# Kernel tuning notes

Measured on AMD Instinct MI355X. Metric: run time of the kernel, lower is better.

The kernel has to match this reference:

```python
import jax, jax.numpy as jnp
import numpy as np

N_NODES = 20000
N_EDGES = 640000
N_TRIP = 1000000
C = 128          # channels
E = 64           # expansion_features
CUTOFF = 5.0
LOG2 = float(np.log(2.0))


def ssp(x):
    # ShiftedSoftplus
    return jax.nn.softplus(x) - LOG2


def setup_inputs() -> dict:
    key = jax.random.key(0)
    ks = jax.random.split(key, 12)
    features = jax.random.normal(ks[0], (N_NODES, C), dtype=jnp.float32)
    neighbour_distances = jax.random.uniform(ks[1], (N_EDGES,), dtype=jnp.float32) * (1.2 * CUTOFF)
    neighbour_list = jax.random.randint(ks[2], (2, N_EDGES), 0, N_NODES, dtype=jnp.int32)
    triplet_idxs = jax.random.randint(ks[3], (N_TRIP, 3), 0, N_NODES, dtype=jnp.int32)
    angles = jax.random.uniform(ks[4], (N_TRIP,), dtype=jnp.float32) * np.pi
    r_ij = jax.random.uniform(ks[5], (N_TRIP,), dtype=jnp.float32) * CUTOFF
    r_ik = jax.random.uniform(ks[6], (N_TRIP,), dtype=jnp.float32) * CUTOFF
    # learned parameters (Linear layers without bias; stored [in, out])
    W_pre = jax.random.normal(ks[7], (C, C), dtype=jnp.float32) / np.sqrt(C)
    W2b1 = jax.random.normal(ks[8], (E, E), dtype=jnp.float32) / np.sqrt(E)
    W2b2 = jax.random.normal(ks[9], (E, C), dtype=jnp.float32) / np.sqrt(E)
    W3b1 = jax.random.normal(ks[10], (3, C // 2), dtype=jnp.float32) / np.sqrt(3.0)
    W3b2 = jax.random.normal(ks[11], (C // 2, C), dtype=jnp.float32) / np.sqrt(C // 2)
    W_post = jax.random.normal(jax.random.fold_in(key, 99), (C, C), dtype=jnp.float32) / np.sqrt(C)
    return {
        "features": features,
        "neighbour_distances": neighbour_distances,
        "neighbour_list": neighbour_list,
        "triplet_idxs": triplet_idxs,
        "angles": angles,
        "r_ij": r_ij,
        "r_ik": r_ik,
        "W_pre": W_pre,
        "W2b1": W2b1,
        "W2b2": W2b2,
        "W3b1": W3b1,
        "W3b2": W3b2,
        "W_post": W_post,
    }


def reference(features, neighbour_distances, neighbour_list, triplet_idxs,
              angles, r_ij, r_ik, W_pre, W2b1, W2b2, W3b1, W3b2, W_post):
    # 1) pre-linear
    h = features @ W_pre                                   # [N, C]

    # 2) radial basis (Gaussian smearing) with smooth cosine cutoff envelope
    centers = jnp.linspace(0.0, CUTOFF, E, dtype=jnp.float32)  # [E]
    width = CUTOFF / E
    gamma = 1.0 / (2.0 * width * width)
    d = neighbour_distances[:, None]                       # [n_edges, 1]
    rb = jnp.exp(-gamma * (d - centers) ** 2)              # [n_edges, E]
    cutoff_mask = (neighbour_distances < CUTOFF).astype(jnp.float32)
    cutoff_values = 0.5 * (1.0 + jnp.cos(np.pi * neighbour_distances / CUTOFF))
    rb = rb * (cutoff_values * cutoff_mask)[:, None]       # fused envelope

    # 3) two-body messages: gather neighbour node features, modulate by radial MLP
    neighbor_h = h[neighbour_list[1]]                      # [n_edges, C]
    two_body = neighbor_h * (ssp(rb @ W2b1) @ W2b2)        # [n_edges, C]

    # 4) three-body messages: angular MLP on (r_ij, r_ik, cos(angle)),
    #    gather node features at triplet_idxs[:,1], scatter-add into edge slots
    tbf = jnp.stack([r_ij, r_ik, jnp.cos(angles)], axis=-1)  # [n_trip, 3]
    w3 = ssp(tbf @ W3b1) @ W3b2                              # [n_trip, C]
    msgs = h[triplet_idxs[:, 1]] * w3                        # [n_trip, C]
    edge_msgs = jnp.zeros_like(two_body).at[triplet_idxs[:, 1]].add(msgs)

    # 5) aggregate messages over neighbours (to central atom = neighbour_list[0])
    messages = two_body + edge_msgs
    agg = jax.ops.segment_sum(messages, neighbour_list[0], num_segments=N_NODES)

    # 6) post-linear
    return agg @ W_post
```

## Files before the change

### kernel.cpp

```cpp
#include <hip/hip_runtime.h>
#include <hip/hip_fp16.h>
#include <math.h>

#define TID threadIdx.x

typedef ushort u16x8 __attribute__((ext_vector_type(8)));
typedef unsigned char uchar;

static constexpr int NN = 20000;
static constexpr int NE = 640000;
static constexpr int NT = 1000000;
static constexpr int C = 128;
static constexpr int E = 64;
static constexpr int LUTN = 4104;
static constexpr int NBKT = 313;
static constexpr int NB2 = 512;
static constexpr int CHE2 = 1250;
static constexpr int CHT2 = 1954;
static constexpr float CUT = 5.0f;
static constexpr float LN2 = 0.69314718055994530942f;

__device__ __forceinline__ float ssp(float x) {
    return fmaxf(x, 0.0f) + __logf(1.0f + __expf(-fabsf(x))) - LN2;
}

__device__ __forceinline__ ushort f2bf(float x) {
    uint u = __float_as_uint(x);
    return (ushort)((u + 0x7FFFu + ((u >> 16) & 1u)) >> 16);
}

__device__ __forceinline__ float bf2f(ushort u) {
    return __uint_as_float((uint)u << 16);
}

__device__ __forceinline__ float h2f(uint bits) {
    return __half2float(__ushort_as_half((ushort)(bits & 0xFFFFu)));
}

__global__ __launch_bounds__(256) void k_gemm16f(const float* __restrict__ A,
                                                 const float* __restrict__ W,
                                                 float* __restrict__ out, int nrows) {
    __shared__ ushort wB[C * C];
    __shared__ float aL[16][132];
    for (int i = TID; i < C * C / 4; i += 256) {
        float4 w4 = ((const float4*)W)[i];
        ushort4 u = {f2bf(w4.x), f2bf(w4.y), f2bf(w4.z), f2bf(w4.w)};
        ((ushort4*)wB)[i] = u;
    }
    const int base = blockIdx.x * 16;
    for (int i = TID; i < 512; i += 256) {
        int r = base + (i >> 5);
        float4 v = (r < nrows) ? ((const float4*)A)[(size_t)r * 32 + (i & 31)]
                               : (float4){0.f, 0.f, 0.f, 0.f};
        *(float4*)&aL[i >> 5][(i & 31) << 2] = v;
    }
    __syncthreads();
    const int rg = TID >> 4;
    const int c8 = (TID & 15) << 3;
    float acc[8] = {0.f, 0.f, 0.f, 0.f, 0.f, 0.f, 0.f, 0.f};
    #pragma unroll 8
    for (int k = 0; k < C; ++k) {
        float a = aL[rg][k];
        u16x8 wv = *(const u16x8*)&wB[k * C + c8];
        #pragma unroll
        for (int j = 0; j < 8; ++j) acc[j] = fmaf(a, bf2f(wv[j]), acc[j]);
    }
    int r = base + rg;
    if (r < nrows) {
        float4 o0 = {acc[0], acc[1], acc[2], acc[3]};
        float4 o1 = {acc[4], acc[5], acc[6], acc[7]};
        *(float4*)&out[(size_t)r * C + c8] = o0;
        *(float4*)&out[(size_t)r * C + c8 + 4] = o1;
    }
}

__global__ __launch_bounds__(256) void k_gemm16b(const float* __restrict__ A,
                                                 const float* __restrict__ W,
                                                 ushort* __restrict__ outB, int nrows) {
    __shared__ ushort wB[C * C];
    __shared__ float aL[16][132];
    for (int i = TID; i < C * C / 4; i += 256) {
        float4 w4 = ((const float4*)W)[i];
        ushort4 u = {f2bf(w4.x), f2bf(w4.y), f2bf(w4.z), f2bf(w4.w)};
        ((ushort4*)wB)[i] = u;
    }
    const int base = blockIdx.x * 16;
    for (int i = TID; i < 512; i += 256) {
        int r = base + (i >> 5);
        float4 v = (r < nrows) ? ((const float4*)A)[(size_t)r * 32 + (i & 31)]
                               : (float4){0.f, 0.f, 0.f, 0.f};
        *(float4*)&aL[i >> 5][(i & 31) << 2] = v;
    }
    __syncthreads();
    const int rg = TID >> 4;
    const int c8 = (TID & 15) << 3;
    float acc[8] = {0.f, 0.f, 0.f, 0.f, 0.f, 0.f, 0.f, 0.f};
    #pragma unroll 8
    for (int k = 0; k < C; ++k) {
        float a = aL[rg][k];
        u16x8 wv = *(const u16x8*)&wB[k * C + c8];
        #pragma unroll
        for (int j = 0; j < 8; ++j) acc[j] = fmaf(a, bf2f(wv[j]), acc[j]);
    }
    int r = base + rg;
    if (r < nrows) {
        u16x8 u;
        #pragma unroll
        for (int j = 0; j < 8; ++j) u[j] = f2bf(acc[j]);
        *(u16x8*)&outB[(size_t)r * C + c8] = u;
    }
}

__global__ __launch_bounds__(256) void k_lut(const float* __restrict__ W2b1,
                                             const float* __restrict__ W2b2,
                                             ushort* __restrict__ lutB,
                                             float2* __restrict__ spLut) {
    if (blockIdx.x == (LUTN + 7) / 8) {
        for (int e = TID; e < 512; e += 256) {
            float t0 = (float)e * (1.0f / 32.0f);
            float t1 = (float)(e + 1) * (1.0f / 32.0f);
            float v0 = log1pf(__expf(-t0));
            float v1 = log1pf(__expf(-t1));
            spLut[e] = make_float2(v0, v1 - v0);
        }
        return;
    }
    __shared__ float w1[E * E];
    __shared__ float w2[E * C];
    __shared__ float rbL[8][E];
    __shared__ float hid[8][E];
    for (int i = TID; i < E * E; i += 256) w1[i] = W2b1[i];
    for (int i = TID; i < E * C; i += 256) w2[i] = W2b2[i];
    const int jj = TID & 63;
    const int esA = TID >> 6;
    const int eg = TID >> 5;
    const int c4 = (TID & 31) << 2;
    const float gamma = 81.92f;
    const float cstep = CUT / 63.0f;
    const float delta = CUT / 4096.0f;
    const int base = blockIdx.x * 8;
    __syncthreads();
    #pragma unroll
    for (int s = 0; s < 2; ++s) {
        int es = esA + 4 * s;
        float d = (float)(base + es) * delta;
        float cv = (d < CUT) ? 0.5f * (1.0f + __cosf((float)M_PI * d / CUT)) : 0.0f;
        float dd = d - (float)jj * cstep;
        rbL[es][jj] = __expf(-gamma * dd * dd) * cv;
    }
    __syncthreads();
    #pragma unroll
    for (int s = 0; s < 2; ++s) {
        int es = esA + 4 * s;
        float a = 0.f;
        #pragma unroll 16
        for (int k = 0; k < E; ++k)
            a = fmaf(rbL[es][k], w1[k * E + jj], a);
        hid[es][jj] = ssp(a);
    }
    __syncthreads();
    float4 o = {0.f, 0.f, 0.f, 0.f};
    #pragma unroll
    for (int j = 0; j < E; ++j) {
        float t = hid[eg][j];
        const float4 w4 = *(const float4*)&w2[j * C + c4];
        o.x = fmaf(t, w4.x, o.x);
        o.y = fmaf(t, w4.y, o.y);
        o.z = fmaf(t, w4.z, o.z);
        o.w = fmaf(t, w4.w, o.w);
    }
    int row = base + eg;
    if (row < LUTN) {
        ushort4 u = {f2bf(o.x), f2bf(o.y), f2bf(o.z), f2bf(o.w)};
        *(ushort4*)&lutB[(size_t)row * C + c4] = u;
    }
}

__global__ __launch_bounds__(256) void k_bcount(const int* __restrict__ nl0,
                                                const int* __restrict__ tidx,
                                                uchar* __restrict__ cntE,
                                                uchar* __restrict__ cntT) {
    __shared__ int h[NBKT];
    const int b = blockIdx.x;
    for (int i = TID; i < NBKT; i += 256) h[i] = 0;
    __syncthreads();
    const int e0 = b * CHE2, e1 = min(e0 + CHE2, NE);
    for (int i = e0 + TID; i < e1; i += 256) atomicAdd(&h[nl0[i] >> 6], 1);
    __syncthreads();
    for (int i = TID; i < NBKT; i += 256) { cntE[(size_t)i * NB2 + b] = (uchar)h[i]; h[i] = 0; }
    __syncthreads();
    const int t0 = b * CHT2, t1 = min(t0 + CHT2, NT);
    for (int i = t0 + TID; i < t1; i += 256) atomicAdd(&h[tidx[3 * i + 1] >> 6], 1);
    __syncthreads();
    for (int i = TID; i < NBKT; i += 256) cntT[(size_t)i * NB2 + b] = (uchar)h[i];
}

__global__ __launch_bounds__(256) void k_bscan(const uchar* __restrict__ cE,
                                               const uchar* __restrict__ cT,
                                               ushort* __restrict__ baseE,
                                               ushort* __restrict__ baseT,
                                               int* __restrict__ totEb,
                                               int* __restrict__ totTb) {
    const int lane = TID & 63;
    const int wv = TID >> 6;
    int task = blockIdx.x * 4 + wv;
    if (task >= 2 * NBKT) return;
    const bool isE = task < NBKT;
    const int k = isE ? task : task - NBKT;
    const uchar* src = isE ? cE : cT;
    ushort* dst = isE ? baseE : baseT;
    int* dT = isE ? totEb : totTb;
    int v[8], pre[8], s = 0;
    #pragma unroll
    for (int j = 0; j < 8; ++j) {
        v[j] = src[(size_t)k * NB2 + lane * 8 + j];
        pre[j] = s;
        s += v[j];
    }
    int incl = s;
    #pragma unroll
    for (int off = 1; off < 64; off <<= 1) {
        int t = __shfl_up(incl, off, 64);
        if (lane >= off) incl += t;
    }
    int excl = incl - s;
    #pragma unroll
    for (int j = 0; j < 8; ++j)
        dst[(size_t)k * NB2 + lane * 8 + j] = (ushort)(excl + pre[j]);
    if (lane == 63) dT[k] = incl;
}

__device__ void scan_one(const int* __restrict__ hist, int* __restrict__ start, int n) {
    __shared__ int wsum[16];
    __shared__ int carryS;
    const int lane = TID & 63;
    const int wv = TID >> 6;
    if (TID == 0) carryS = 0;
    __syncthreads();
    for (int base = 0; base < n; base += 1024) {
        int i = base + TID;
        int v = (i < n) ? hist[i] : 0;
        int acc = v;
        #pragma unroll
        for (int off = 1; off < 64; off <<= 1) {
            int t = __shfl_up(acc, off, 64);
            if (lane >= off) acc += t;
        }
        if (lane == 63) wsum[wv] = acc;
        __syncthreads();
        int woff = 0;
        for (int w = 0; w < wv; ++w) woff += wsum[w];
        int excl = carryS + woff + acc - v;
        if (i < n) start[i] = excl;
        __syncthreads();
        if (TID == 1023) carryS = excl + v;
        __syncthreads();
    }
}

__global__ __launch_bounds__(1024) void k_bktscan(const int* __restrict__ totEb, int* __restrict__ bksE,
                                                  const int* __restrict__ totTb, int* __restrict__ bksT) {
    if (blockIdx.x == 0) scan_one(totEb, bksE, NBKT);
    else                 scan_one(totTb, bksT, NBKT);
}

__global__ __launch_bounds__(256) void k_bplace(const int* __restrict__ nl0,
                                                const int* __restrict__ nl1,
                                                const float* __restrict__ dist,
                                                const int* __restrict__ tidx,
                                                const float* __restrict__ angles,
                                                const float* __restrict__ rij,
                                                const float* __restrict__ rik,
                                                const ushort* __restrict__ baseE,
                                                const ushort* __restrict__ baseT,
                                                const int* __restrict__ bksE,
                                                const int* __restrict__ bksT,
                                                int2* __restrict__ eT,
                                                int2* __restrict__ tT) {
    __shared__ int cur[NBKT];
    const int b = blockIdx.x;
    for (int k = TID; k < NBKT; k += 256)
        cur[k] = bksE[k] + (int)baseE[(size_t)k * NB2 + b];
    __syncthreads();
    const int e0 = b * CHE2, e1 = min(e0 + CHE2, NE);
    for (int i = e0 + TID; i < e1; i += 256) {
        int n0 = nl0[i];
        int pos = atomicAdd(&cur[n0 >> 6], 1);
        uint tq = (uint)fmaf(dist[i], 209715.2f, 0.5f);
        eT[pos] = make_int2((int)(tq | ((uint)(n0 & 63) << 26)), nl1[i]);
    }
    __syncthreads();
    for (int k = TID; k < NBKT; k += 256)
        cur[k] = bksT[k] + (int)baseT[(size_t)k * NB2 + b];
    __syncthreads();
    const int t0 = b * CHT2, tEnd = min(t0 + CHT2, NT);
    for (int i = t0 + TID; i < tEnd; i += 256) {
        int t1 = tidx[3 * i + 1];
        int pos = atomicAdd(&cur[t1 >> 6], 1);
        uint ab = ((uint)__half_as_ushort(__float2half_rn(rik[i])) << 16)
                | (uint)__half_as_ushort(__float2half_rn(rij[i]));
        uint cc = (uint)__half_as_ushort(__float2half_rn(__cosf(angles[i])))
                | ((uint)(t1 & 63) << 16);
        tT[pos] = make_int2((int)ab, (int)cc);
    }
}

__global__ __launch_bounds__(256) void k_nsort(const int2* __restrict__ eTs,
                                               const int2* __restrict__ tTs,
                                               const int* __restrict__ bksE,
                                               const int* __restrict__ bksT,
                                               const int* __restrict__ totEb,
                                               const int* __restrict__ totTb,
                                               int2* __restrict__ eS,
                                               int2* __restrict__ tS,
                                               int* __restrict__ startE,
                                               int* __restrict__ totE,
                                               int* __restrict__ startT,
                                               int* __restrict__ totT) {
    __shared__ int hist[64];
    __shared__ int cur[64];
    const bool isE = blockIdx.x < NBKT;
    const int bkt = isE ? blockIdx.x : blockIdx.x - NBKT;
    const int2* src = isE ? eTs : tTs;
    int2* dst = isE ? eS : tS;
    const int s0 = isE ? bksE[bkt] : bksT[bkt];
    const int cnt = isE ? totEb[bkt] : totTb[bkt];
    int* stX = isE ? startE : startT;
    int* ttX = isE ? totE : totT;
    if (TID < 64) hist[TID] = 0;
    __syncthreads();
    for (int i = TID; i < cnt; i += 256) {
        int2 p = src[s0 + i];
        int nlo = isE ? (int)(((uint)p.x >> 26) & 63u) : (int)(((uint)p.y >> 16) & 63u);
        atomicAdd(&hist[nlo], 1);
    }
    __syncthreads();
    if (TID < 64) {
        int v = hist[TID];
        int incl = v;
        #pragma unroll
        for (int off = 1; off < 64; off <<= 1) {
            int t = __shfl_up(incl, off, 64);
            if (TID >= off) incl += t;
        }
        int excl = incl - v;
        cur[TID] = s0 + excl;
        int node = bkt * 64 + TID;
        if (node < NN) { stX[node] = s0 + excl; ttX[node] = v; }
    }
    __syncthreads();
    for (int i = TID; i < cnt; i += 256) {
        int2 p = src[s0 + i];
        int nlo = isE ? (int)(((uint)p.x >> 26) & 63u) : (int)(((uint)p.y >> 16) & 63u);
        int pos = atomicAdd(&cur[nlo], 1);
        dst[pos] = p;
    }
}

__global__ __launch_bounds__(256) void k_edges_node(const int2* __restrict__ eS,
                                                    const int* __restrict__ startE,
                                                    const int* __restrict__ totE,
                                                    const ushort* __restrict__ hB,
                                                    const ushort* __restrict__ lutB,
                                                    float* __restrict__ agg) {
    __shared__ int4 stage[4][64];
    const int lane = TID & 63;
    const int wv = TID >> 6;
    const int c2b = lane << 2;
    for (int r = blockIdx.x * 4 + wv; r < NN; r += gridDim.x * 4) {
        const int s0 = startE[r];
        const int cnt = totE[r];
        float a0 = 0.f, a1 = 0.f;
        for (int base = 0; base < cnt; base += 64) {
            const int n = min(64, cnt - base);
            if (lane < n) {
                int2 p = eS[s0 + base + lane];
                uint tq = ((uint)p.x) & 0x03FFFFFFu;
                int idx = min((int)(tq >> 8), LUTN - 2);
                float fr = (float)(tq & 255u) * (1.0f / 256.0f);
                stage[wv][lane] = make_int4(idx * (C * 2), __float_as_int(fr),
                                            p.y * (C * 2), 0);
            }
            asm volatile("s_waitcnt lgkmcnt(0)" ::: "memory");
            #pragma unroll 8
            for (int i = 0; i < n; ++i) {
                int4 q = stage[wv][i];
                float fr = __int_as_float(q.y);
                ushort2 A2 = *(const ushort2*)((const char*)lutB + q.x + c2b);
                ushort2 B2 = *(const ushort2*)((const char*)lutB + q.x + 256 + c2b);
                ushort2 H2 = *(const ushort2*)((const char*)hB + q.z + c2b);
                float ax = bf2f(A2.x), ay = bf2f(A2.y);
                float ox = fmaf(fr, bf2f(B2.x) - ax, ax);
                float oy = fmaf(fr, bf2f(B2.y) - ay, ay);
                a0 = fmaf(ox, bf2f(H2.x), a0);
                a1 = fmaf(oy, bf2f(H2.y), a1);
            }
            asm volatile("s_waitcnt lgkmcnt(0)" ::: "memory");
        }
        float2 o = {a0, a1};
        *(float2*)&agg[(size_t)r * C + (lane << 1)] = o;
    }
}

__global__ __launch_bounds__(256) void k_trip_node(const int* __restrict__ startT,
                                                   const int* __restrict__ totT,
                                                   const int2* __restrict__ tS,
                                                   const float* __restrict__ W3b1,
                                                   const float* __restrict__ W3b2,
                                                   const float2* __restrict__ spLut,
                                                   const ushort* __restrict__ hB,
                                                   const int* __restrict__ nl0,
                                                   float* __restrict__ agg) {
    __shared__ uint w2p[64 * 64];
    __shared__ float2 spl[512];
    __shared__ float4 stage[4][64];
    for (int i = TID; i < 512; i += 256) spl[i] = spLut[i];
    for (int i = TID; i < 4096; i += 256) {
        int k = i >> 6, l = i & 63;
        float lo = W3b2[k * C + l];
        float hi = W3b2[k * C + 64 + l];
        w2p[i] = ((uint)f2bf(hi) << 16) | (uint)f2bf(lo);
    }
    __syncthreads();
    const int lane = TID & 63;
    const int wv = TID >> 6;
    const float w1a = W3b1[lane];
    const float w1b = W3b1[64 + lane];
    const float w1c = W3b1[128 + lane];
    for (int r = blockIdx.x * 4 + wv; r < NN; r += gridDim.x * 4) {
        const int s0 = startT[r];
        const int cnt = totT[r];
        float usum = 0.f;
        for (int base = 0; base < cnt; base += 64) {
            const int n = min(64, cnt - base);
            if (lane < n) {
                uint2 p = ((const uint2*)tS)[s0 + base + lane];
                float4 f;
                f.x = h2f(p.x);
                f.y = h2f(p.x >> 16);
                f.z = h2f(p.y);
                f.w = 0.f;
                stage[wv][lane] = f;
            }
            asm volatile("s_waitcnt lgkmcnt(0)" ::: "memory");
            #pragma unroll 4
            for (int i = 0; i < n; ++i) {
                float4 p = stage[wv][i];
                float x = fmaf(p.x, w1a, fmaf(p.y, w1b, p.z * w1c));
                float t = fabsf(x) * 32.0f;
                int idx = min((int)t, 511);
                float fr = t - (float)idx;
                float2 vs = spl[idx];
                usum += fmaxf(x, 0.f) + fmaf(fr, vs.y, vs.x);
            }
            asm volatile("s_waitcnt lgkmcnt(0)" ::: "memory");
        }
        usum -= LN2 * (float)cnt;
        float o0 = 0.f, o1 = 0.f;
        #pragma unroll 8
        for (int k = 0; k < 64; ++k) {
            float uk = __shfl(usum, k, 64);
            uint wp = w2p[k * 64 + lane];
            float lo = __uint_as_float(wp << 16);
            float hi = __uint_as_float(wp & 0xFFFF0000u);
            o0 = fmaf(uk, lo, o0);
            o1 = fmaf(uk, hi, o1);
        }
        const int n0 = nl0[r];
        float h0 = bf2f(hB[(size_t)r * C + lane]);
        float h1 = bf2f(hB[(size_t)r * C + 64 + lane]);
        unsafeAtomicAdd(&agg[(size_t)n0 * C + lane], o0 * h0);
        unsafeAtomicAdd(&agg[(size_t)n0 * C + 64 + lane], o1 * h1);
    }
}

extern "C" void kernel_launch(void* const* d_in, const int* in_sizes, int n_in,
                              void* d_out, int out_size, void* d_ws, size_t ws_size,
                              hipStream_t stream) {
    const float* features = (const float*)d_in[0];
    const float* ndist    = (const float*)d_in[1];
    const int*   nlist    = (const int*)d_in[2];
    const int*   tidx     = (const int*)d_in[3];
    const float* angles   = (const float*)d_in[4];
    const float* rij      = (const float*)d_in[5];
    const float* rik      = (const float*)d_in[6];
    const float* W_pre    = (const float*)d_in[7];
    const float* W2b1     = (const float*)d_in[8];
    const float* W2b2     = (const float*)d_in[9];
    const float* W3b1     = (const float*)d_in[10];
    const float* W3b2     = (const float*)d_in[11];
    const float* W_post   = (const float*)d_in[12];
    float* out = (float*)d_out;

    char* w = (char*)d_ws;
    float* agg    = (float*)w;
    int2* eT      = (int2*)w;
    w += (size_t)NN * C * 4;
    ushort* hB    = (ushort*)w;  w += (size_t)NN * C * 2;
    ushort* lutB  = (ushort*)w;  w += (size_t)LUTN * C * 2;
    int2* eS      = (int2*)w;    w += (size_t)NE * 8;
    int2* tS      = (int2*)w;    w += (size_t)NT * 8;
    int2* tT      = (int2*)w;    w += (size_t)NT * 8;
    uchar* cntE   = (uchar*)w;   w += (size_t)NBKT * NB2;
    uchar* cntT   = (uchar*)w;   w += (size_t)NBKT * NB2;
    ushort* baseE = (ushort*)w;  w += (size_t)NBKT * NB2 * 2;
    ushort* baseT = (ushort*)w;  w += (size_t)NBKT * NB2 * 2;
    int* totEb    = (int*)w;     w += 1280;
    int* totTb    = (int*)w;     w += 1280;
    int* bksE     = (int*)w;     w += 1280;
    int* bksT     = (int*)w;     w += 1280;
    int* startE   = (int*)w;     w += (size_t)NN * 4;
    int* totE     = (int*)w;     w += (size_t)NN * 4;
    int* startT   = (int*)w;     w += (size_t)NN * 4;
    int* totT     = (int*)w;     w += (size_t)NN * 4;
    float2* spLut = (float2*)w;  w += 512 * 8;

    const int* nl0 = nlist;
    const int* nl1 = nlist + NE;

    hipLaunchKernelGGL(k_gemm16b, dim3((NN + 15) / 16), dim3(256), 0, stream,
                       features, W_pre, hB, NN);
    hipLaunchKernelGGL(k_lut, dim3((LUTN + 7) / 8 + 1), dim3(256), 0, stream,
                       W2b1, W2b2, lutB, spLut);
    hipLaunchKernelGGL(k_bcount, dim3(NB2), dim3(256), 0, stream,
                       nl0, tidx, cntE, cntT);
    hipLaunchKernelGGL(k_bscan, dim3((2 * NBKT + 3) / 4), dim3(256), 0, stream,
                       cntE, cntT, baseE, baseT, totEb, totTb);
    hipLaunchKernelGGL(k_bktscan, dim3(2), dim3(1024), 0, stream,
                       totEb, bksE, totTb, bksT);
    hipLaunchKernelGGL(k_bplace, dim3(NB2), dim3(256), 0, stream,
                       nl0, nl1, ndist, tidx, angles, rij, rik,
                       baseE, baseT, bksE, bksT, eT, tT);
    hipLaunchKernelGGL(k_nsort, dim3(2 * NBKT), dim3(256), 0, stream,
                       eT, tT, bksE, bksT, totEb, totTb,
                       eS, tS, startE, totE, startT, totT);
    hipLaunchKernelGGL(k_edges_node, dim3(2500), dim3(256), 0, stream,
                       eS, startE, totE, hB, lutB, agg);
    hipLaunchKernelGGL(k_trip_node, dim3(2500), dim3(256), 0, stream,
                       startT, totT, tS, W3b1, W3b2, spLut, hB, nl0, agg);
    hipLaunchKernelGGL(k_gemm16f, dim3((NN + 15) / 16), dim3(256), 0, stream,
                       agg, W_post, out, NN);
}
```

Baseline: 192.0 us.

## Double-buffer staged edge/triplet chunks with register prefetch and split accumulators

Both node-aggregation kernels now prefetch the next 64-entry chunk of sorted edge/triplet records into registers while the current chunk is processed. They stage chunks into a double-buffered LDS slot, which removes the trailing wait per chunk. The triplet kernel packs its softplus LUT to bf16 pairs, halving LDS footprint, and uses two independent accumulators to shorten the dependency chain. Grid sizes for both kernels are reduced. The bf16 softplus LUT adds some precision loss, and relying on lgkmcnt waits with slot alternation assumes same-wave ordering.

New measurement: 193.4 us. Within noise of the previous version (+0.7%).

```diff
diff --git a/kernel.cpp b/kernel.cpp
--- a/kernel.cpp
+++ b/kernel.cpp
@@ -363,7 +363,7 @@
                                                     const ushort* __restrict__ hB,
                                                     const ushort* __restrict__ lutB,
                                                     float* __restrict__ agg) {
-    __shared__ int4 stage[4][64];
+    __shared__ int4 stage[4][2][64];
     const int lane = TID & 63;
     const int wv = TID >> 6;
     const int c2b = lane << 2;
@@ -371,20 +371,26 @@
         const int s0 = startE[r];
         const int cnt = totE[r];
         float a0 = 0.f, a1 = 0.f;
-        for (int base = 0; base < cnt; base += 64) {
+        int2 pf;
+        if (lane < min(64, cnt)) pf = eS[s0 + lane];
+        const int nch = (cnt + 63) >> 6;
+        for (int c = 0; c < nch; ++c) {
+            const int base = c << 6;
             const int n = min(64, cnt - base);
+            const int slot = c & 1;
             if (lane < n) {
-                int2 p = eS[s0 + base + lane];
-                uint tq = ((uint)p.x) & 0x03FFFFFFu;
+                uint tq = ((uint)pf.x) & 0x03FFFFFFu;
                 int idx = min((int)(tq >> 8), LUTN - 2);
                 float fr = (float)(tq & 255u) * (1.0f / 256.0f);
-                stage[wv][lane] = make_int4(idx * (C * 2), __float_as_int(fr),
-                                            p.y * (C * 2), 0);
+                stage[wv][slot][lane] = make_int4(idx * (C * 2), __float_as_int(fr),
+                                                  pf.y * (C * 2), 0);
             }
+            int nb = base + 64;
+            if (nb < cnt && lane < cnt - nb) pf = eS[s0 + nb + lane];
             asm volatile("s_waitcnt lgkmcnt(0)" ::: "memory");
             #pragma unroll 8
             for (int i = 0; i < n; ++i) {
-                int4 q = stage[wv][i];
+                int4 q = stage[wv][slot][i];
                 float fr = __int_as_float(q.y);
                 ushort2 A2 = *(const ushort2*)((const char*)lutB + q.x + c2b);
                 ushort2 B2 = *(const ushort2*)((const char*)lutB + q.x + 256 + c2b);
@@ -395,8 +401,8 @@
                 a0 = fmaf(ox, bf2f(H2.x), a0);
                 a1 = fmaf(oy, bf2f(H2.y), a1);
             }
-            asm volatile("s_waitcnt lgkmcnt(0)" ::: "memory");
         }
+        asm volatile("s_waitcnt lgkmcnt(0)" ::: "memory");
         float2 o = {a0, a1};
         *(float2*)&agg[(size_t)r * C + (lane << 1)] = o;
     }
@@ -412,14 +418,15 @@
                                                    const int* __restrict__ nl0,
                                                    float* __restrict__ agg) {
     __shared__ uint w2p[64 * 64];
-    __shared__ float2 spl[512];
-    __shared__ float4 stage[4][64];
-    for (int i = TID; i < 512; i += 256) spl[i] = spLut[i];
+    __shared__ uint spl[512];
+    __shared__ float4 stage[4][2][64];
+    for (int i = TID; i < 512; i += 256) {
+        float2 vs = spLut[i];
+        spl[i] = ((uint)f2bf(vs.y) << 16) | (uint)f2bf(vs.x);
+    }
     for (int i = TID; i < 4096; i += 256) {
         int k = i >> 6, l = i & 63;
-        float lo = W3b2[k * C + l];
-        float hi = W3b2[k * C + 64 + l];
-        w2p[i] = ((uint)f2bf(hi) << 16) | (uint)f2bf(lo);
+        w2p[i] = ((uint)f2bf(W3b2[k * C + 64 + l]) << 16) | (uint)f2bf(W3b2[k * C + l]);
     }
     __syncthreads();
     const int lane = TID & 63;
@@ -430,41 +437,62 @@
     for (int r = blockIdx.x * 4 + wv; r < NN; r += gridDim.x * 4) {
         const int s0 = startT[r];
         const int cnt = totT[r];
-        float usum = 0.f;
-        for (int base = 0; base < cnt; base += 64) {
+        float usA = 0.f, usB = 0.f;
+        uint2 pf;
+        if (lane < min(64, cnt)) pf = ((const uint2*)tS)[s0 + lane];
+        const int nch = (cnt + 63) >> 6;
+        for (int c = 0; c < nch; ++c) {
+            const int base = c << 6;
             const int n = min(64, cnt - base);
+            const int slot = c & 1;
             if (lane < n) {
-                uint2 p = ((const uint2*)tS)[s0 + base + lane];
                 float4 f;
-                f.x = h2f(p.x);
-                f.y = h2f(p.x >> 16);
-                f.z = h2f(p.y);
+                f.x = h2f(pf.x);
+                f.y = h2f(pf.x >> 16);
+                f.z = h2f(pf.y);
                 f.w = 0.f;
-                stage[wv][lane] = f;
+                stage[wv][slot][lane] = f;
             }
+            int nb = base + 64;
+            if (nb < cnt && lane < cnt - nb) pf = ((const uint2*)tS)[s0 + nb + lane];
             asm volatile("s_waitcnt lgkmcnt(0)" ::: "memory");
+            int i = 0;
             #pragma unroll 4
-            for (int i = 0; i < n; ++i) {
-                float4 p = stage[wv][i];
-                float x = fmaf(p.x, w1a, fmaf(p.y, w1b, p.z * w1c));
-                float t = fabsf(x) * 32.0f;
-                int idx = min((int)t, 511);
-                float fr = t - (float)idx;
-                float2 vs = spl[idx];
-                usum += fmaxf(x, 0.f) + fmaf(fr, vs.y, vs.x);
+            for (; i + 1 < n; i += 2) {
+                float4 pa = stage[wv][slot][i];
+                float4 pb = stage[wv][slot][i + 1];
+                float xa = fmaf(pa.x, w1a, fmaf(pa.y, w1b, pa.z * w1c));
+                float xb = fmaf(pb.x, w1a, fmaf(pb.y, w1b, pb.z * w1c));
+                float ta = fabsf(xa) * 32.0f;
+                float tb = fabsf(xb) * 32.0f;
+                int ia = min((int)ta, 511);
+                int ib = min((int)tb, 511);
+                float fa = ta - (float)ia;
+                float fb = tb - (float)ib;
+                uint va = spl[ia];
+                uint vb = spl[ib];
+                usA += fmaxf(xa, 0.f) + fmaf(fa, bf2f((ushort)(va >> 16)), bf2f((ushort)va));
+                usB += fmaxf(xb, 0.f) + fmaf(fb, bf2f((ushort)(vb >> 16)), bf2f((ushort)vb));
             }
-            asm volatile("s_waitcnt lgkmcnt(0)" ::: "memory");
+            if (i < n) {
+                float4 pa = stage[wv][slot][i];
+                float xa = fmaf(pa.x, w1a, fmaf(pa.y, w1b, pa.z * w1c));
+                float ta = fabsf(xa) * 32.0f;
+                int ia = min((int)ta, 511);
+                float fa = ta - (float)ia;
+                uint va = spl[ia];
+                usA += fmaxf(xa, 0.f) + fmaf(fa, bf2f((ushort)(va >> 16)), bf2f((ushort)va));
+            }
         }
-        usum -= LN2 * (float)cnt;
+        asm volatile("s_waitcnt lgkmcnt(0)" ::: "memory");
+        float usum = usA + usB - LN2 * (float)cnt;
         float o0 = 0.f, o1 = 0.f;
         #pragma unroll 8
         for (int k = 0; k < 64; ++k) {
             float uk = __shfl(usum, k, 64);
             uint wp = w2p[k * 64 + lane];
-            float lo = __uint_as_float(wp << 16);
-            float hi = __uint_as_float(wp & 0xFFFF0000u);
-            o0 = fmaf(uk, lo, o0);
-            o1 = fmaf(uk, hi, o1);
+            o0 = fmaf(uk, __uint_as_float(wp << 16), o0);
+            o1 = fmaf(uk, __uint_as_float(wp & 0xFFFF0000u), o1);
         }
         const int n0 = nl0[r];
         float h0 = bf2f(hB[(size_t)r * C + lane]);
@@ -534,9 +562,9 @@
     hipLaunchKernelGGL(k_nsort, dim3(2 * NBKT), dim3(256), 0, stream,
                        eT, tT, bksE, bksT, totEb, totTb,
                        eS, tS, startE, totE, startT, totT);
-    hipLaunchKernelGGL(k_edges_node, dim3(2500), dim3(256), 0, stream,
+    hipLaunchKernelGGL(k_edges_node, dim3(2048), dim3(256), 0, stream,
                        eS, startE, totE, hB, lutB, agg);
-    hipLaunchKernelGGL(k_trip_node, dim3(2500), dim3(256), 0, stream,
+    hipLaunchKernelGGL(k_trip_node, dim3(1536), dim3(256), 0, stream,
                        startT, totT, tS, W3b1, W3b2, spLut, hB, nl0, agg);
     hipLaunchKernelGGL(k_gemm16f, dim3((NN + 15) / 16), dim3(256), 0, stream,
                        agg, W_post, out, NN);
```
